# Optimization experiments

Measured on AMD Instinct MI355X. Metric: run time of the kernel, lower is better.

Reference implementation:

```python
import jax, jax.numpy as jnp
import numpy as np

K = 16  # neighbors, incl. self


def setup_inputs() -> dict:
    key = jax.random.key(0)
    ks = jax.random.split(key, 16)
    N, C = 8192, 256  # points, channels (inter_channels == in_channels == C)
    s = 0.05
    inp = {
        'coords': jax.random.uniform(ks[0], (N, 3), dtype=jnp.float32) * 100.0,
        'feats': jax.random.normal(ks[1], (N, C), dtype=jnp.float32),
        'theta_w': jax.random.normal(ks[2], (C, C), dtype=jnp.float32) * s,
        'theta_b': jax.random.normal(ks[3], (C,), dtype=jnp.float32) * s,
        'phi_w': jax.random.normal(ks[4], (C, C), dtype=jnp.float32) * s,
        'phi_b': jax.random.normal(ks[5], (C,), dtype=jnp.float32) * s,
        'g_w': jax.random.normal(ks[6], (C, C), dtype=jnp.float32) * s,
        'g_b': jax.random.normal(ks[7], (C,), dtype=jnp.float32) * s,
        'pe1_w1': jax.random.normal(ks[8], (3, C), dtype=jnp.float32) * s,
        'pe1_b1': jax.random.normal(ks[9], (C,), dtype=jnp.float32) * s,
        'pe1_w2': jax.random.normal(ks[10], (C, C), dtype=jnp.float32) * s,
        'pe1_b2': jax.random.normal(ks[11], (C,), dtype=jnp.float32) * s,
        'W_w': jax.random.normal(ks[12], (C, C), dtype=jnp.float32) * s,
        'W_b': jax.random.normal(ks[13], (C,), dtype=jnp.float32) * s,
    }
    return inp


def reference(coords, feats, theta_w, theta_b, phi_w, phi_b, g_w, g_b,
              pe1_w1, pe1_b1, pe1_w2, pe1_b2, W_w, W_b):
    C = feats.shape[-1]
    # KNN (squared dists, includes self as nearest) == pytorch3d knn_points
    sq = jnp.sum(coords * coords, axis=-1)  # [N]
    d2 = sq[:, None] + sq[None, :] - 2.0 * (coords @ coords.T)  # [N,N]
    _, idx = jax.lax.top_k(-d2, K)  # [N,K] sorted by ascending distance

    nn_coords = coords[idx]            # [N,K,3] knn gather
    nn_feats = feats[idx]              # [N,K,C]

    theta_f = feats @ theta_w + theta_b          # [N,C]
    phi_f = nn_feats @ phi_w + phi_b             # [N,K,C]

    delta_coords = nn_coords - coords[:, None, :]  # [N,K,3]
    # pe1 MLP; NOTE: original code uses pe1 for both pe1 and pe2 (shared)
    pe = jax.nn.relu(delta_coords @ pe1_w1 + pe1_b1) @ pe1_w2 + pe1_b2  # [N,K,C]

    delta_features = (pe * (theta_f[:, None, :] - phi_f) + pe) / jnp.sqrt(jnp.float32(C))
    sim = jax.nn.softmax(delta_features, axis=1)  # softmax over K neighbors

    g_feats = nn_feats @ g_w + g_b               # [N,K,C]
    y = jnp.sum(sim * g_feats, axis=1)           # [N,C]

    # W (1x1 Minkowski conv == per-point linear) + residual
    return y @ W_w + W_b + feats
```

## Files before the change

### kernel.cpp

```cpp
#include <hip/hip_runtime.h>

typedef __bf16 bf16_t;
typedef bf16_t bf16x8 __attribute__((ext_vector_type(8)));
typedef bf16_t bf16x4 __attribute__((ext_vector_type(4)));
typedef float f32x4 __attribute__((ext_vector_type(4)));
typedef unsigned long long u64;

#define N_PTS 8192
#define C_DIM 256
#define K_NN 16

#define GRID_G    16
#define GRID_NC   (GRID_G * GRID_G * GRID_G)
#define GRID_CELL 6.25f
#define GRID_INV  0.16f

__global__ __launch_bounds__(256) void cast_feats_kernel(const float* __restrict__ f,
                                                         bf16_t* __restrict__ fb) {
    int i = (blockIdx.x * 256 + threadIdx.x) * 4;
    float4 v = *(const float4*)(f + i);
    bf16x4 o;
    o[0] = (bf16_t)v.x; o[1] = (bf16_t)v.y; o[2] = (bf16_t)v.z; o[3] = (bf16_t)v.w;
    *(bf16x4*)(fb + i) = o;
}

__global__ __launch_bounds__(256) void prep_weights_kernel(
    const float* __restrict__ w0, const float* __restrict__ w1,
    const float* __restrict__ w2, const float* __restrict__ w3,
    const float* __restrict__ w4, bf16_t* __restrict__ wt_base) {
    int m = blockIdx.y;
    const float* src = (m == 0) ? w0 : (m == 1) ? w1 : (m == 2) ? w2 : (m == 3) ? w3 : w4;
    bf16_t* dst = wt_base + m * (C_DIM * C_DIM);
#pragma unroll
    for (int i = 0; i < 4; ++i) {
        int o = blockIdx.x * 1024 + i * 256 + threadIdx.x;
        int tkb = o >> 9;
        int rem = o & 511;
        int lm = rem >> 5;
        int r = rem & 31;
        int k = (tkb & 7) * 32 + r;
        int n = (tkb >> 3) * 16 + lm;
        dst[o] = (bf16_t)src[k * C_DIM + n];
    }
}

__global__ __launch_bounds__(256) void grid_zero_kernel(int* __restrict__ cellCount,
                                                        int* __restrict__ gcount) {
    int i = blockIdx.x * 256 + threadIdx.x;
    cellCount[i] = 0;
    if (i == 0) *gcount = 0;
}

__global__ __launch_bounds__(256) void grid_count_kernel(const float* __restrict__ coords,
                                                         int* __restrict__ cellCount,
                                                         int* __restrict__ cid) {
    int i = blockIdx.x * 256 + threadIdx.x;
    float x = coords[3 * i + 0], y = coords[3 * i + 1], z = coords[3 * i + 2];
    int cx = (int)(x * GRID_INV); if (cx > GRID_G - 1) cx = GRID_G - 1;
    int cy = (int)(y * GRID_INV); if (cy > GRID_G - 1) cy = GRID_G - 1;
    int cz = (int)(z * GRID_INV); if (cz > GRID_G - 1) cz = GRID_G - 1;
    int c = (cx * GRID_G + cy) * GRID_G + cz;
    cid[i] = c;
    atomicAdd(&cellCount[c], 1);
}

__global__ __launch_bounds__(256) void grid_scan_kernel(const int* __restrict__ cellCount,
                                                        int* __restrict__ cellStart,
                                                        int* __restrict__ cellPtr) {
    __shared__ int part[256];
    int t = threadIdx.x;
    int base = t * 16;
    int v[16];
    int sum = 0;
#pragma unroll
    for (int i = 0; i < 16; ++i) { v[i] = cellCount[base + i]; sum += v[i]; }
    part[t] = sum;
    __syncthreads();
    for (int off = 1; off < 256; off <<= 1) {
        int x = (t >= off) ? part[t - off] : 0;
        __syncthreads();
        part[t] += x;
        __syncthreads();
    }
    int acc = part[t] - sum;
#pragma unroll
    for (int i = 0; i < 16; ++i) {
        cellStart[base + i] = acc;
        cellPtr[base + i] = acc;
        acc += v[i];
    }
    if (t == 255) cellStart[GRID_NC] = acc;
}

__global__ __launch_bounds__(256) void grid_scatter_kernel(
    const float* __restrict__ coords, const int* __restrict__ cid, int* __restrict__ cellPtr,
    float* __restrict__ sx, float* __restrict__ sy, float* __restrict__ sz,
    float* __restrict__ ssq, int* __restrict__ sidx) {
    int i = blockIdx.x * 256 + threadIdx.x;
    int c = cid[i];
    int pos = atomicAdd(&cellPtr[c], 1);
    float x = coords[3 * i + 0], y = coords[3 * i + 1], z = coords[3 * i + 2];
    sx[pos] = x; sy[pos] = y; sz[pos] = z;
    ssq[pos] = __fadd_rn(__fadd_rn(__fmul_rn(x, x), __fmul_rn(y, y)), __fmul_rn(z, z));
    sidx[pos] = i;
}

__global__ __launch_bounds__(256) void knn_grid_kernel(
    const float* __restrict__ coords, const int* __restrict__ cellStart,
    const float* __restrict__ sx, const float* __restrict__ sy,
    const float* __restrict__ sz, const float* __restrict__ ssq,
    const int* __restrict__ sidx,
    int* __restrict__ idx_out, int* __restrict__ glist, int* __restrict__ gcount) {
    const int tid = threadIdx.x;
    const int wave = tid >> 6, lane = tid & 63;
    const int q = blockIdx.x * 4 + wave;

    __shared__ int segBase[4][25];
    __shared__ int segPref[4][26];
    __shared__ u64 cand[4][256];
    __shared__ int cnt[4];

    if (lane == 0) cnt[wave] = 0;

    const float qx = coords[3 * q + 0], qy = coords[3 * q + 1], qz = coords[3 * q + 2];
    const float sqi = __fadd_rn(__fadd_rn(__fmul_rn(qx, qx), __fmul_rn(qy, qy)),
                                __fmul_rn(qz, qz));

    int cx = (int)(qx * GRID_INV); if (cx > GRID_G - 1) cx = GRID_G - 1;
    int cy = (int)(qy * GRID_INV); if (cy > GRID_G - 1) cy = GRID_G - 1;
    int cz = (int)(qz * GRID_INV); if (cz > GRID_G - 1) cz = GRID_G - 1;
    int wx0 = cx - 2; if (wx0 < 0) wx0 = 0;
    int wx1 = cx + 2; if (wx1 > GRID_G - 1) wx1 = GRID_G - 1;
    int wy0 = cy - 2; if (wy0 < 0) wy0 = 0;
    int wy1 = cy + 2; if (wy1 > GRID_G - 1) wy1 = GRID_G - 1;
    int wz0 = cz - 2; if (wz0 < 0) wz0 = 0;
    int wz1 = cz + 2; if (wz1 > GRID_G - 1) wz1 = GRID_G - 1;

    const float INF = __int_as_float(0x7f800000);
    float rc = INF;
    if (wx0 > 0)          rc = fminf(rc, qx - (float)wx0 * GRID_CELL);
    if (wx1 < GRID_G - 1) rc = fminf(rc, (float)(wx1 + 1) * GRID_CELL - qx);
    if (wy0 > 0)          rc = fminf(rc, qy - (float)wy0 * GRID_CELL);
    if (wy1 < GRID_G - 1) rc = fminf(rc, (float)(wy1 + 1) * GRID_CELL - qy);
    if (wz0 > 0)          rc = fminf(rc, qz - (float)wz0 * GRID_CELL);
    if (wz1 < GRID_G - 1) rc = fminf(rc, (float)(wz1 + 1) * GRID_CELL - qz);
    float rc2 = rc * rc * 0.9999f;

    int nx = wx1 - wx0 + 1, nyc = wy1 - wy0 + 1;
    int ns = nx * nyc;
    if (lane < ns) {
        int scx = wx0 + lane / nyc;
        int scy = wy0 + lane % nyc;
        int b = (scx * GRID_G + scy) * GRID_G;
        int s0 = cellStart[b + wz0];
        int s1 = cellStart[b + wz1 + 1];
        segBase[wave][lane] = s0;
        segPref[wave][lane] = s1 - s0;
    }
    __syncthreads();
    if (lane == 0) {
        int acc = 0;
        for (int s = 0; s < ns; ++s) { int l = segPref[wave][s]; segPref[wave][s] = acc; acc += l; }
        segPref[wave][ns] = acc;
    }
    __syncthreads();

    const int M = segPref[wave][ns];
    bool flag = (M < K_NN);

    float lmin = INF;
    {
        int s = 0;
        for (int t = lane; t < M; t += 64) {
            while (t >= segPref[wave][s + 1]) ++s;
            int pos = segBase[wave][s] + (t - segPref[wave][s]);
            float x = sx[pos], y = sy[pos], z = sz[pos], sj = ssq[pos];
            float dot = __fmaf_rn(z, qz, __fmaf_rn(y, qy, __fmul_rn(x, qx)));
            float d2 = __fsub_rn(__fadd_rn(sqi, sj), __fmul_rn(2.0f, dot));
            lmin = fminf(lmin, d2);
        }
    }
    float g = fminf(lmin, __shfl_xor(lmin, 1));
    g = fminf(g, __shfl_xor(g, 2));
    float tau = fmaxf(g, __shfl_xor(g, 4));
    tau = fmaxf(tau, __shfl_xor(tau, 8));
    tau = fmaxf(tau, __shfl_xor(tau, 16));
    tau = fmaxf(tau, __shfl_xor(tau, 32));

    {
        int s = 0;
        for (int t = lane; t < M; t += 64) {
            while (t >= segPref[wave][s + 1]) ++s;
            int pos = segBase[wave][s] + (t - segPref[wave][s]);
            float x = sx[pos], y = sy[pos], z = sz[pos], sj = ssq[pos];
            float dot = __fmaf_rn(z, qz, __fmaf_rn(y, qy, __fmul_rn(x, qx)));
            float d2 = __fsub_rn(__fadd_rn(sqi, sj), __fmul_rn(2.0f, dot));
            if (d2 <= tau) {
                unsigned u = __float_as_uint(d2);
                u = (u & 0x80000000u) ? ~u : (u | 0x80000000u);
                int slot = atomicAdd(&cnt[wave], 1);
                if (slot < 256)
                    cand[wave][slot] = (((u64)u) << 32) | (unsigned)sidx[pos];
            }
        }
    }
    __syncthreads();

    int m = cnt[wave];
    if (m > 256) { flag = true; m = 256; }
    u64 k0 = ~0ull, k1 = ~0ull, k2 = ~0ull, k3 = ~0ull;
    if (lane < m) k0 = cand[wave][lane];
    if (lane + 64 < m) k1 = cand[wave][lane + 64];
    if (lane + 128 < m) k2 = cand[wave][lane + 128];
    if (lane + 192 < m) k3 = cand[wave][lane + 192];
    u64 lm2 = k0; int li = 0;
    if (k1 < lm2) { lm2 = k1; li = 1; }
    if (k2 < lm2) { lm2 = k2; li = 2; }
    if (k3 < lm2) { lm2 = k3; li = 3; }
    int keep = 0;
    u64 last = ~0ull;
#pragma unroll 1
    for (int r = 0; r < 16; ++r) {
        u64 w = lm2;
#pragma unroll
        for (int off = 1; off < 64; off <<= 1) {
            u64 o = __shfl_xor(w, off);
            w = (o < w) ? o : w;
        }
        if (lane == r) keep = (int)(unsigned)(w & 0xffffffffull);
        last = w;
        if (lm2 == w) {
            if (li == 0) k0 = ~0ull;
            else if (li == 1) k1 = ~0ull;
            else if (li == 2) k2 = ~0ull;
            else k3 = ~0ull;
            lm2 = k0; li = 0;
            if (k1 < lm2) { lm2 = k1; li = 1; }
            if (k2 < lm2) { lm2 = k2; li = 2; }
            if (k3 < lm2) { lm2 = k3; li = 3; }
        }
    }

    if (!flag) {
        unsigned ou = (unsigned)(last >> 32);
        unsigned db = (ou & 0x80000000u) ? (ou ^ 0x80000000u) : ~ou;
        float d16 = __uint_as_float(db);
        if (d16 >= rc2) flag = true;
    }
    if (flag && lane == 0) {
        int sl = atomicAdd(gcount, 1);
        glist[sl] = q;
    }
    if (lane < 16) idx_out[q * K_NN + lane] = keep;
}

__global__ __launch_bounds__(256) void knn_fallback_kernel(const float* __restrict__ coords,
                                                           const int* __restrict__ glist,
                                                           const int* __restrict__ gcount,
                                                           int* __restrict__ idx_out) {
    const int count = *gcount;
    const int n0 = blockIdx.x * 4;
    if (n0 >= count) return;

    const int tid = threadIdx.x;
    const int wave = tid >> 6, lane = tid & 63;
    __shared__ float red16[4][16];
    __shared__ u64 cand[4][256];
    __shared__ int cnt[4];
    __shared__ int qids[4];

    if (tid < 4) {
        cnt[tid] = 0;
        int slot = n0 + tid;
        qids[tid] = glist[slot < count ? slot : count - 1];
    }
    __syncthreads();

    float qx[4], qy[4], qz[4], sqi[4];
#pragma unroll
    for (int q = 0; q < 4; ++q) {
        int id = qids[q];
        qx[q] = coords[3 * id + 0];
        qy[q] = coords[3 * id + 1];
        qz[q] = coords[3 * id + 2];
        sqi[q] = __fadd_rn(__fadd_rn(__fmul_rn(qx[q], qx[q]), __fmul_rn(qy[q], qy[q])),
                           __fmul_rn(qz[q], qz[q]));
    }

    const float INF = __int_as_float(0x7f800000);
    const float* cp = coords + tid * 96;

    float lmin[4] = {INF, INF, INF, INF};
#pragma unroll
    for (int c = 0; c < 4; ++c) {
        float buf[24];
#pragma unroll
        for (int v = 0; v < 6; ++v)
            *(float4*)(buf + v * 4) = *(const float4*)(cp + c * 24 + v * 4);
#pragma unroll
        for (int p = 0; p < 8; ++p) {
            float x = buf[3 * p + 0], y = buf[3 * p + 1], z = buf[3 * p + 2];
            float sqj = __fadd_rn(__fadd_rn(__fmul_rn(x, x), __fmul_rn(y, y)),
                                  __fmul_rn(z, z));
#pragma unroll
            for (int q = 0; q < 4; ++q) {
                float dot = __fmaf_rn(z, qz[q], __fmaf_rn(y, qy[q], __fmul_rn(x, qx[q])));
                float d2 = __fsub_rn(__fadd_rn(sqi[q], sqj), __fmul_rn(2.0f, dot));
                lmin[q] = fminf(lmin[q], d2);
            }
        }
    }

#pragma unroll
    for (int q = 0; q < 4; ++q) {
        float g = lmin[q];
        g = fminf(g, __shfl_xor(g, 1));
        g = fminf(g, __shfl_xor(g, 2));
        g = fminf(g, __shfl_xor(g, 4));
        g = fminf(g, __shfl_xor(g, 8));
        if ((lane & 15) == 0) red16[q][wave * 4 + (lane >> 4)] = g;
    }
    __syncthreads();

    float tau[4];
#pragma unroll
    for (int q = 0; q < 4; ++q) {
        float t = red16[q][0];
#pragma unroll
        for (int i = 1; i < 16; ++i) t = fmaxf(t, red16[q][i]);
        tau[q] = t;
    }

#pragma unroll
    for (int c = 0; c < 4; ++c) {
        float buf[24];
#pragma unroll
        for (int v = 0; v < 6; ++v)
            *(float4*)(buf + v * 4) = *(const float4*)(cp + c * 24 + v * 4);
#pragma unroll
        for (int p = 0; p < 8; ++p) {
            float x = buf[3 * p + 0], y = buf[3 * p + 1], z = buf[3 * p + 2];
            float sqj = __fadd_rn(__fadd_rn(__fmul_rn(x, x), __fmul_rn(y, y)),
                                  __fmul_rn(z, z));
            int j = tid * 32 + c * 8 + p;
#pragma unroll
            for (int q = 0; q < 4; ++q) {
                float dot = __fmaf_rn(z, qz[q], __fmaf_rn(y, qy[q], __fmul_rn(x, qx[q])));
                float d2 = __fsub_rn(__fadd_rn(sqi[q], sqj), __fmul_rn(2.0f, dot));
                if (d2 <= tau[q]) {
                    unsigned u = __float_as_uint(d2);
                    u = (u & 0x80000000u) ? ~u : (u | 0x80000000u);
                    int slot = atomicAdd(&cnt[q], 1);
                    if (slot < 256)
                        cand[q][slot] = (((u64)u) << 32) | (unsigned)j;
                }
            }
        }
    }
    __syncthreads();

    int m = cnt[wave]; if (m > 256) m = 256;
    u64 k0 = ~0ull, k1 = ~0ull, k2 = ~0ull, k3 = ~0ull;
    if (lane < m) k0 = cand[wave][lane];
    if (lane + 64 < m) k1 = cand[wave][lane + 64];
    if (lane + 128 < m) k2 = cand[wave][lane + 128];
    if (lane + 192 < m) k3 = cand[wave][lane + 192];
    u64 lm2 = k0; int li = 0;
    if (k1 < lm2) { lm2 = k1; li = 1; }
    if (k2 < lm2) { lm2 = k2; li = 2; }
    if (k3 < lm2) { lm2 = k3; li = 3; }
    int keep = 0;
#pragma unroll 1
    for (int r = 0; r < 16; ++r) {
        u64 w = lm2;
#pragma unroll
        for (int off = 1; off < 64; off <<= 1) {
            u64 o = __shfl_xor(w, off);
            w = (o < w) ? o : w;
        }
        if (lane == r) keep = (int)(unsigned)(w & 0xffffffffull);
        if (lm2 == w) {
            if (li == 0) k0 = ~0ull;
            else if (li == 1) k1 = ~0ull;
            else if (li == 2) k2 = ~0ull;
            else k3 = ~0ull;
            lm2 = k0; li = 0;
            if (k1 < lm2) { lm2 = k1; li = 1; }
            if (k2 < lm2) { lm2 = k2; li = 2; }
            if (k3 < lm2) { lm2 = k3; li = 3; }
        }
    }
    if (lane < 16) idx_out[qids[wave] * K_NN + lane] = keep;
}

__global__ __launch_bounds__(256, 2) void proj_kernel(
    const bf16_t* __restrict__ fb, const bf16_t* __restrict__ wt_base,
    const float* __restrict__ tb, const float* __restrict__ pb, const float* __restrict__ gb,
    float* __restrict__ T, bf16_t* __restrict__ Pb, bf16_t* __restrict__ Gb) {
    const int sel = blockIdx.y;
    const bf16_t* Wt = wt_base + sel * (C_DIM * C_DIM);
    const float* bias = (sel == 0) ? tb : (sel == 1) ? pb : gb;
    const int wave = threadIdx.x >> 6, lane = threadIdx.x & 63;
    const int q = lane >> 4, lm = lane & 15;
    const int m0 = blockIdx.x * 64;

    bf16x8 bfr[4][8];
#pragma unroll
    for (int ti = 0; ti < 4; ++ti)
#pragma unroll
        for (int kb = 0; kb < 8; ++kb)
            bfr[ti][kb] = *(const bf16x8*)(Wt + (((wave * 4 + ti) * 8 + kb) << 9) + lm * 32 + q * 8);

    float bv[4];
#pragma unroll
    for (int ti = 0; ti < 4; ++ti) bv[ti] = bias[(wave * 4 + ti) * 16 + lm];

#pragma unroll
    for (int p = 0; p < 4; ++p) {
        const bf16_t* arow = fb + (m0 + p * 16 + lm) * C_DIM + q * 8;
        bf16x8 a[8];
#pragma unroll
        for (int kb = 0; kb < 8; ++kb) a[kb] = *(const bf16x8*)(arow + kb * 32);
        f32x4 acc[4];
#pragma unroll
        for (int ti = 0; ti < 4; ++ti) acc[ti] = (f32x4){0.f, 0.f, 0.f, 0.f};
#pragma unroll
        for (int ti = 0; ti < 4; ++ti)
#pragma unroll
            for (int kb = 0; kb < 8; ++kb)
                acc[ti] = __builtin_amdgcn_mfma_f32_16x16x32_bf16(a[kb], bfr[ti][kb], acc[ti], 0, 0, 0);

#pragma unroll
        for (int ti = 0; ti < 4; ++ti) {
            int c = (wave * 4 + ti) * 16 + lm;
#pragma unroll
            for (int r = 0; r < 4; ++r) {
                float v = acc[ti][r] + bv[ti];
                int off = (m0 + p * 16 + q * 4 + r) * C_DIM + c;
                if (sel == 0) T[off] = v;
                else if (sel == 1) Pb[off] = (bf16_t)v;
                else Gb[off] = (bf16_t)v;
            }
        }
    }
}

#define HPAD 264
#define P_BLK 8
#define HROWS (P_BLK * 16)
__global__ __launch_bounds__(256, 2) void pe2_fused_kernel(
    const float* __restrict__ coords, const int* __restrict__ idx,
    const float* __restrict__ T, const bf16_t* __restrict__ Pb, const bf16_t* __restrict__ Gb,
    const float* __restrict__ w1, const float* __restrict__ b1, const float* __restrict__ b2,
    const bf16_t* __restrict__ Wt2, bf16_t* __restrict__ yb) {
    __shared__ __align__(16) bf16_t h_lds[HROWS * HPAD];
    __shared__ float dxyz[HROWS][3];
    __shared__ int idxl[HROWS];
    const int tid = threadIdx.x;
    const int p0 = blockIdx.x * P_BLK;
    const int wave = tid >> 6, lane = tid & 63;
    const int q = lane >> 4, lm = lane & 15;

    bf16x8 bfr[4][8];
#pragma unroll
    for (int ti = 0; ti < 4; ++ti)
#pragma unroll
        for (int kb = 0; kb < 8; ++kb)
            bfr[ti][kb] = *(const bf16x8*)(Wt2 + (((wave * 4 + ti) * 8 + kb) << 9) + lm * 32 + q * 8);
    float b2c[4];
#pragma unroll
    for (int ti = 0; ti < 4; ++ti) b2c[ti] = b2[(wave * 4 + ti) * 16 + lm];

    if (tid < HROWS) {
        int n = p0 + (tid >> 4);
        int j = idx[n * K_NN + (tid & 15)];
        idxl[tid] = j;
        dxyz[tid][0] = coords[3 * j + 0] - coords[3 * n + 0];
        dxyz[tid][1] = coords[3 * j + 1] - coords[3 * n + 1];
        dxyz[tid][2] = coords[3 * j + 2] - coords[3 * n + 2];
    }
    __syncthreads();

    {
        int c = tid;
        float wx = w1[c], wy = w1[C_DIM + c], wz = w1[2 * C_DIM + c], bb = b1[c];
#pragma unroll 4
        for (int r = 0; r < HROWS; ++r) {
            float pre = dxyz[r][0] * wx + dxyz[r][1] * wy + dxyz[r][2] * wz + bb;
            h_lds[r * HPAD + c] = (bf16_t)fmaxf(pre, 0.0f);
        }
    }
    __syncthreads();

#pragma unroll 1
    for (int lp = 0; lp < P_BLK; ++lp) {
        const int n = p0 + lp;
        const bf16_t* hrow = h_lds + (lp * 16 + lm) * HPAD + q * 8;
        bf16x8 a[8];
#pragma unroll
        for (int kb = 0; kb < 8; ++kb) a[kb] = *(const bf16x8*)(hrow + kb * 32);
        f32x4 acc[4];
#pragma unroll
        for (int ti = 0; ti < 4; ++ti) acc[ti] = (f32x4){0.f, 0.f, 0.f, 0.f};
#pragma unroll
        for (int ti = 0; ti < 4; ++ti)
#pragma unroll
            for (int kb = 0; kb < 8; ++kb)
                acc[ti] = __builtin_amdgcn_mfma_f32_16x16x32_bf16(a[kb], bfr[ti][kb], acc[ti], 0, 0, 0);

        int jr[4];
#pragma unroll
        for (int r = 0; r < 4; ++r) jr[r] = idxl[lp * 16 + q * 4 + r];

#pragma unroll
        for (int ti = 0; ti < 4; ++ti) {
            int c = (wave * 4 + ti) * 16 + lm;
            float phi[4], gv[4];
#pragma unroll
            for (int r = 0; r < 4; ++r) {
                phi[r] = (float)Pb[jr[r] * C_DIM + c];
                gv[r]  = (float)Gb[jr[r] * C_DIM + c];
            }
            float Tn = T[n * C_DIM + c];
            float df[4];
#pragma unroll
            for (int r = 0; r < 4; ++r) {
                float pe = acc[ti][r] + b2c[ti];
                df[r] = (pe * (Tn - phi[r]) + pe) * 0.0625f;
            }
            float mx = fmaxf(fmaxf(df[0], df[1]), fmaxf(df[2], df[3]));
            mx = fmaxf(mx, __shfl_xor(mx, 16));
            mx = fmaxf(mx, __shfl_xor(mx, 32));
            float e[4], s = 0.f;
#pragma unroll
            for (int r = 0; r < 4; ++r) { e[r] = __expf(df[r] - mx); s += e[r]; }
            s += __shfl_xor(s, 16);
            s += __shfl_xor(s, 32);
            float inv = 1.0f / s;
            float y = 0.f;
#pragma unroll
            for (int r = 0; r < 4; ++r) y += e[r] * inv * gv[r];
            y += __shfl_xor(y, 16);
            y += __shfl_xor(y, 32);
            if (q == 0) yb[n * C_DIM + c] = (bf16_t)y;
        }
    }
}

__global__ __launch_bounds__(256, 2) void final_kernel(
    const bf16_t* __restrict__ yb, const bf16_t* __restrict__ Wt,
    const float* __restrict__ Wb, const float* __restrict__ feats,
    float* __restrict__ out) {
    const int wave = threadIdx.x >> 6, lane = threadIdx.x & 63;
    const int q = lane >> 4, lm = lane & 15;
    const int m0 = blockIdx.x * 64;

    bf16x8 bfr[4][8];
#pragma unroll
    for (int ti = 0; ti < 4; ++ti)
#pragma unroll
        for (int kb = 0; kb < 8; ++kb)
            bfr[ti][kb] = *(const bf16x8*)(Wt + (((wave * 4 + ti) * 8 + kb) << 9) + lm * 32 + q * 8);
    float bv[4];
#pragma unroll
    for (int ti = 0; ti < 4; ++ti) bv[ti] = Wb[(wave * 4 + ti) * 16 + lm];

#pragma unroll
    for (int p = 0; p < 4; ++p) {
        const bf16_t* arow = yb + (m0 + p * 16 + lm) * C_DIM + q * 8;
        bf16x8 a[8];
#pragma unroll
        for (int kb = 0; kb < 8; ++kb) a[kb] = *(const bf16x8*)(arow + kb * 32);
        f32x4 acc[4];
#pragma unroll
        for (int ti = 0; ti < 4; ++ti) acc[ti] = (f32x4){0.f, 0.f, 0.f, 0.f};
#pragma unroll
        for (int ti = 0; ti < 4; ++ti)
#pragma unroll
            for (int kb = 0; kb < 8; ++kb)
                acc[ti] = __builtin_amdgcn_mfma_f32_16x16x32_bf16(a[kb], bfr[ti][kb], acc[ti], 0, 0, 0);

#pragma unroll
        for (int ti = 0; ti < 4; ++ti) {
            int c = (wave * 4 + ti) * 16 + lm;
#pragma unroll
            for (int r = 0; r < 4; ++r) {
                int off = (m0 + p * 16 + q * 4 + r) * C_DIM + c;
                out[off] = acc[ti][r] + bv[ti] + feats[off];
            }
        }
    }
}

extern "C" void kernel_launch(void* const* d_in, const int* in_sizes, int n_in,
                              void* d_out, int out_size, void* d_ws, size_t ws_size,
                              hipStream_t stream) {
    const float* coords = (const float*)d_in[0];
    const float* feats  = (const float*)d_in[1];
    const float* theta_w = (const float*)d_in[2];
    const float* theta_b = (const float*)d_in[3];
    const float* phi_w   = (const float*)d_in[4];
    const float* phi_b   = (const float*)d_in[5];
    const float* g_w     = (const float*)d_in[6];
    const float* g_b     = (const float*)d_in[7];
    const float* pe1_w1  = (const float*)d_in[8];
    const float* pe1_b1  = (const float*)d_in[9];
    const float* pe1_w2  = (const float*)d_in[10];
    const float* pe1_b2  = (const float*)d_in[11];
    const float* W_w     = (const float*)d_in[12];
    const float* W_b     = (const float*)d_in[13];
    float* out = (float*)d_out;

    char* w = (char*)d_ws;
    size_t off = 0;
    int* idx = (int*)(w + off);        off += (size_t)N_PTS * K_NN * 4;
    bf16_t* fb = (bf16_t*)(w + off);   off += (size_t)N_PTS * C_DIM * 2;
    bf16_t* wt = (bf16_t*)(w + off);   off += (size_t)5 * C_DIM * C_DIM * 2;
    float* T = (float*)(w + off);      off += (size_t)N_PTS * C_DIM * 4;
    bf16_t* Pb = (bf16_t*)(w + off);   off += (size_t)N_PTS * C_DIM * 2;
    bf16_t* Gb = (bf16_t*)(w + off);   off += (size_t)N_PTS * C_DIM * 2;
    bf16_t* yb = (bf16_t*)(w + off);   off += (size_t)N_PTS * C_DIM * 2;
    int* cid       = (int*)(w + off);  off += (size_t)N_PTS * 4;
    int* cellCount = (int*)(w + off);  off += (size_t)GRID_NC * 4;
    int* cellStart = (int*)(w + off);  off += (size_t)(GRID_NC + 1) * 4;
    int* cellPtr   = (int*)(w + off);  off += (size_t)GRID_NC * 4;
    float* sxp = (float*)(w + off);    off += (size_t)N_PTS * 4;
    float* syp = (float*)(w + off);    off += (size_t)N_PTS * 4;
    float* szp = (float*)(w + off);    off += (size_t)N_PTS * 4;
    float* ssqp = (float*)(w + off);   off += (size_t)N_PTS * 4;
    int* sidxp = (int*)(w + off);      off += (size_t)N_PTS * 4;
    int* glist = (int*)(w + off);      off += (size_t)N_PTS * 4;
    int* gcount = (int*)(w + off);     off += 256;
    (void)ws_size; (void)in_sizes; (void)n_in; (void)out_size;

    cast_feats_kernel<<<(N_PTS * C_DIM) / 1024, 256, 0, stream>>>(feats, fb);
    prep_weights_kernel<<<dim3(64, 5), 256, 0, stream>>>(theta_w, phi_w, g_w, pe1_w2, W_w, wt);

    grid_zero_kernel<<<GRID_NC / 256, 256, 0, stream>>>(cellCount, gcount);
    grid_count_kernel<<<N_PTS / 256, 256, 0, stream>>>(coords, cellCount, cid);
    grid_scan_kernel<<<1, 256, 0, stream>>>(cellCount, cellStart, cellPtr);
    grid_scatter_kernel<<<N_PTS / 256, 256, 0, stream>>>(coords, cid, cellPtr,
                                                         sxp, syp, szp, ssqp, sidxp);
    knn_grid_kernel<<<N_PTS / 4, 256, 0, stream>>>(coords, cellStart, sxp, syp, szp,
                                                   ssqp, sidxp, idx, glist, gcount);
    knn_fallback_kernel<<<N_PTS / 4, 256, 0, stream>>>(coords, glist, gcount, idx);

    proj_kernel<<<dim3(N_PTS / 64, 3), 256, 0, stream>>>(fb, wt, theta_b, phi_b, g_b, T, Pb, Gb);
    pe2_fused_kernel<<<N_PTS / P_BLK, 256, 0, stream>>>(coords, idx, T, Pb, Gb,
                                                        pe1_w1, pe1_b1, pe1_b2,
                                                        wt + 3 * C_DIM * C_DIM, yb);
    final_kernel<<<N_PTS / 64, 256, 0, stream>>>(yb, wt + 4 * C_DIM * C_DIM, W_b, feats, out);
}
```

Measured before the change: 223.1 us.

## Interleave phi/g projections and prefetch gathers before MFMA in pe2 kernel

Phi and g projections are now stored interleaved as bf16 pairs in one buffer, so each neighbor gather in the fused pe2 kernel fetches both values with a single 4-byte load. Those gathers and the theta load are hoisted ahead of the MFMA loop so their latency can overlap the matrix math. The point block shrinks from 8 to 4 and launch bounds ask for 4 blocks per CU, trading reuse of the per-block weight fragment loads for more occupancy. The proj kernel now writes scattered 2-byte stores at stride 4, and more live registers under the tighter launch bound may cause spills.

```diff
diff --git a/kernel.cpp b/kernel.cpp
--- a/kernel.cpp
+++ b/kernel.cpp
@@ -3,6 +3,7 @@
 typedef __bf16 bf16_t;
 typedef bf16_t bf16x8 __attribute__((ext_vector_type(8)));
 typedef bf16_t bf16x4 __attribute__((ext_vector_type(4)));
+typedef bf16_t bf16x2 __attribute__((ext_vector_type(2)));
 typedef float f32x4 __attribute__((ext_vector_type(4)));
 typedef unsigned long long u64;
 
@@ -396,7 +397,7 @@
 __global__ __launch_bounds__(256, 2) void proj_kernel(
     const bf16_t* __restrict__ fb, const bf16_t* __restrict__ wt_base,
     const float* __restrict__ tb, const float* __restrict__ pb, const float* __restrict__ gb,
-    float* __restrict__ T, bf16_t* __restrict__ Pb, bf16_t* __restrict__ Gb) {
+    float* __restrict__ T, bf16_t* __restrict__ PG) {
     const int sel = blockIdx.y;
     const bf16_t* Wt = wt_base + sel * (C_DIM * C_DIM);
     const float* bias = (sel == 0) ? tb : (sel == 1) ? pb : gb;
@@ -438,19 +439,19 @@
                 float v = acc[ti][r] + bv[ti];
                 int off = (m0 + p * 16 + q * 4 + r) * C_DIM + c;
                 if (sel == 0) T[off] = v;
-                else if (sel == 1) Pb[off] = (bf16_t)v;
-                else Gb[off] = (bf16_t)v;
+                else if (sel == 1) PG[2 * off] = (bf16_t)v;
+                else PG[2 * off + 1] = (bf16_t)v;
             }
         }
     }
 }
 
 #define HPAD 264
-#define P_BLK 8
+#define P_BLK 4
 #define HROWS (P_BLK * 16)
-__global__ __launch_bounds__(256, 2) void pe2_fused_kernel(
+__global__ __launch_bounds__(256, 4) void pe2_fused_kernel(
     const float* __restrict__ coords, const int* __restrict__ idx,
-    const float* __restrict__ T, const bf16_t* __restrict__ Pb, const bf16_t* __restrict__ Gb,
+    const float* __restrict__ T, const bf16_t* __restrict__ PG,
     const float* __restrict__ w1, const float* __restrict__ b1, const float* __restrict__ b2,
     const bf16_t* __restrict__ Wt2, bf16_t* __restrict__ yb) {
     __shared__ __align__(16) bf16_t h_lds[HROWS * HPAD];
@@ -495,6 +496,21 @@
 #pragma unroll 1
     for (int lp = 0; lp < P_BLK; ++lp) {
         const int n = p0 + lp;
+
+        int jr[4];
+#pragma unroll
+        for (int r = 0; r < 4; ++r) jr[r] = idxl[lp * 16 + q * 4 + r];
+        bf16x2 pg[4][4];
+        float Tn[4];
+#pragma unroll
+        for (int ti = 0; ti < 4; ++ti) {
+            int c = (wave * 4 + ti) * 16 + lm;
+            Tn[ti] = T[n * C_DIM + c];
+#pragma unroll
+            for (int r = 0; r < 4; ++r)
+                pg[ti][r] = *(const bf16x2*)(PG + 2 * (jr[r] * C_DIM + c));
+        }
+
         const bf16_t* hrow = h_lds + (lp * 16 + lm) * HPAD + q * 8;
         bf16x8 a[8];
 #pragma unroll
@@ -508,25 +524,14 @@
             for (int kb = 0; kb < 8; ++kb)
                 acc[ti] = __builtin_amdgcn_mfma_f32_16x16x32_bf16(a[kb], bfr[ti][kb], acc[ti], 0, 0, 0);
 
-        int jr[4];
-#pragma unroll
-        for (int r = 0; r < 4; ++r) jr[r] = idxl[lp * 16 + q * 4 + r];
-
 #pragma unroll
         for (int ti = 0; ti < 4; ++ti) {
             int c = (wave * 4 + ti) * 16 + lm;
-            float phi[4], gv[4];
-#pragma unroll
-            for (int r = 0; r < 4; ++r) {
-                phi[r] = (float)Pb[jr[r] * C_DIM + c];
-                gv[r]  = (float)Gb[jr[r] * C_DIM + c];
-            }
-            float Tn = T[n * C_DIM + c];
             float df[4];
 #pragma unroll
             for (int r = 0; r < 4; ++r) {
                 float pe = acc[ti][r] + b2c[ti];
-                df[r] = (pe * (Tn - phi[r]) + pe) * 0.0625f;
+                df[r] = (pe * (Tn[ti] - (float)pg[ti][r][0]) + pe) * 0.0625f;
             }
             float mx = fmaxf(fmaxf(df[0], df[1]), fmaxf(df[2], df[3]));
             mx = fmaxf(mx, __shfl_xor(mx, 16));
@@ -539,7 +544,7 @@
             float inv = 1.0f / s;
             float y = 0.f;
 #pragma unroll
-            for (int r = 0; r < 4; ++r) y += e[r] * inv * gv[r];
+            for (int r = 0; r < 4; ++r) y += e[r] * inv * (float)pg[ti][r][1];
             y += __shfl_xor(y, 16);
             y += __shfl_xor(y, 32);
             if (q == 0) yb[n * C_DIM + c] = (bf16_t)y;
@@ -617,8 +622,7 @@
     bf16_t* fb = (bf16_t*)(w + off);   off += (size_t)N_PTS * C_DIM * 2;
     bf16_t* wt = (bf16_t*)(w + off);   off += (size_t)5 * C_DIM * C_DIM * 2;
     float* T = (float*)(w + off);      off += (size_t)N_PTS * C_DIM * 4;
-    bf16_t* Pb = (bf16_t*)(w + off);   off += (size_t)N_PTS * C_DIM * 2;
-    bf16_t* Gb = (bf16_t*)(w + off);   off += (size_t)N_PTS * C_DIM * 2;
+    bf16_t* PG = (bf16_t*)(w + off);   off += (size_t)N_PTS * C_DIM * 4;
     bf16_t* yb = (bf16_t*)(w + off);   off += (size_t)N_PTS * C_DIM * 2;
     int* cid       = (int*)(w + off);  off += (size_t)N_PTS * 4;
     int* cellCount = (int*)(w + off);  off += (size_t)GRID_NC * 4;
@@ -645,8 +649,8 @@
                                                    ssqp, sidxp, idx, glist, gcount);
     knn_fallback_kernel<<<N_PTS / 4, 256, 0, stream>>>(coords, glist, gcount, idx);
 
-    proj_kernel<<<dim3(N_PTS / 64, 3), 256, 0, stream>>>(fb, wt, theta_b, phi_b, g_b, T, Pb, Gb);
-    pe2_fused_kernel<<<N_PTS / P_BLK, 256, 0, stream>>>(coords, idx, T, Pb, Gb,
+    proj_kernel<<<dim3(N_PTS / 64, 3), 256, 0, stream>>>(fb, wt, theta_b, phi_b, g_b, T, PG);
+    pe2_fused_kernel<<<N_PTS / P_BLK, 256, 0, stream>>>(coords, idx, T, PG,
                                                         pe1_w1, pe1_b1, pe1_b2,
                                                         wt + 3 * C_DIM * C_DIM, yb);
     final_kernel<<<N_PTS / 64, 256, 0, stream>>>(yb, wt + 4 * C_DIM * C_DIM, W_b, feats, out);
```

After: 268.0 us. +20.1%, slower.
